# Optimization experiments

Measured on AMD Instinct MI355X. Metric: run time of the kernel, lower is better.

The kernel has to match this reference:

```python
import jax, jax.numpy as jnp
import numpy as np

S = 4096   # decoder sequence length
T = 4096   # encoder sequence length
D = 2048   # x_size == qk_size (required for q @ k^T to typecheck)


def setup_inputs() -> dict:
    key = jax.random.key(0)
    k1, k2, k3, k4 = jax.random.split(key, 4)
    x_vectors = jax.random.normal(k1, (S, D), dtype=jnp.float32)
    enc_output = jax.random.normal(k2, (2, T, S), dtype=jnp.float32) * 0.02
    Wq = jax.random.normal(k3, (D, D), dtype=jnp.float32) * 0.02
    bq = jax.random.normal(k4, (D,), dtype=jnp.float32) * 0.02
    return {"x_vectors": x_vectors, "enc_output": enc_output, "Wq": Wq, "bq": bq}


def reference(x_vectors, enc_output, Wq, bq):
    # q = Linear(x): [S, D]
    q = x_vectors @ Wq.T + bq
    # k, v produced by matmul of encoder-output matrices with x: [T, D]
    k = enc_output[0] @ x_vectors
    v = enc_output[1] @ x_vectors
    # attention scores [S, T], scaled by sqrt(qk_size)
    e = (q @ k.T) / jnp.sqrt(jnp.float32(D))
    # softmax over dim=1 (last axis of the rank-2 score matrix)
    a = jax.nn.softmax(e, axis=1)
    # z = a @ v^T: [S, D]
    z = a @ v
    return z
```

## Files before the change

### kernel.cpp

```cpp
#include <hip/hip_runtime.h>


typedef __attribute__((ext_vector_type(8))) __bf16 bf16x8;
typedef __attribute__((ext_vector_type(4))) float f32x4;
typedef __attribute__((ext_vector_type(4))) unsigned short ushort4v;
typedef __attribute__((ext_vector_type(8))) unsigned short ushort8v;

#define S_DIM 4096
#define T_DIM 4096
#define D_DIM 2048

__device__ __forceinline__ unsigned short f2bf(float f) {
    unsigned int u = __float_as_uint(f);
    u += 0x7fffu + ((u >> 16) & 1u);
    return (unsigned short)(u >> 16);
}

__device__ __forceinline__ void block_sync() {
    __builtin_amdgcn_sched_barrier(0);
    __builtin_amdgcn_s_barrier();
    __builtin_amdgcn_sched_barrier(0);
}

#define GL(gptr, sptr)                                                        \
    __builtin_amdgcn_global_load_lds(                                         \
        (__attribute__((address_space(1))) void*)(void*)(gptr),               \
        (__attribute__((address_space(3))) void*)(sptr), 16, 0, 0)

__device__ __forceinline__ f32x4 MFMA(bf16x8 a, bf16x8 b, f32x4 c) {
    return __builtin_amdgcn_mfma_f32_16x16x32_bf16(a, b, c, 0, 0, 0);
}

__global__ __launch_bounds__(256)
void k_convert(const float* __restrict__ in, unsigned short* __restrict__ out, long n) {
    long i = ((long)blockIdx.x * blockDim.x + threadIdx.x) * 8;
    const long stride = (long)gridDim.x * blockDim.x * 8;
    for (; i < n; i += stride) {
        float4 a = *(const float4*)(in + i);
        float4 b = *(const float4*)(in + i + 4);
        ushort8v o;
        o[0] = f2bf(a.x); o[1] = f2bf(a.y); o[2] = f2bf(a.z); o[3] = f2bf(a.w);
        o[4] = f2bf(b.x); o[5] = f2bf(b.y); o[6] = f2bf(b.z); o[7] = f2bf(b.w);
        *(ushort8v*)(out + i) = o;
    }
}

__global__ __launch_bounds__(256)
void k_transpose(const float* __restrict__ in, unsigned short* __restrict__ out,
                 int R, int C) {
    __shared__ float tile[32][33];
    const int bx = blockIdx.x * 32;
    const int by = blockIdx.y * 32;
    const int tx = threadIdx.x;
    const int ty = threadIdx.y;
    #pragma unroll
    for (int i = 0; i < 32; i += 8)
        tile[ty + i][tx] = in[(long)(by + ty + i) * C + bx + tx];
    __syncthreads();
    #pragma unroll
    for (int i = 0; i < 32; i += 8)
        out[(long)(bx + ty + i) * R + by + tx] = f2bf(tile[tx][ty + i]);
}

__global__ __launch_bounds__(256)
void k_transpose_bf(const unsigned short* __restrict__ in,
                    unsigned short* __restrict__ out, int R, int C) {
    __shared__ unsigned short tile[32][33];
    const int bx = blockIdx.x * 32;
    const int by = blockIdx.y * 32;
    const int tx = threadIdx.x;
    const int ty = threadIdx.y;
    #pragma unroll
    for (int i = 0; i < 32; i += 8)
        tile[ty + i][tx] = in[(long)(by + ty + i) * C + bx + tx];
    __syncthreads();
    #pragma unroll
    for (int i = 0; i < 32; i += 8)
        out[(long)(bx + ty + i) * R + by + tx] = tile[tx][ty + i];
}

template<int MFR, bool DOSTG, bool DOREAD, int WVM, bool DOBAR, int LPTA>
__device__ __forceinline__ void seg_t(
    const unsigned short* (&gA)[2], const int (&ldA)[2],
    const unsigned short* (&gB)[2], const int (&ldB)[2],
    char* cur, char* nxt, char* stg, int arB, int brB,
    bf16x8 (&au)[4], bf16x8 (&bu)[4], bf16x8 (&af)[4], bf16x8 (&bf_)[4],
    f32x4 (&acc)[MFR][4])
{
    bf16x8 a47[4];
    if constexpr (MFR == 8) {
        #pragma unroll
        for (int j = 0; j < 4; ++j)
            a47[j] = *(const bf16x8*)(cur + arB + (4 + j) * 1024);
    }
    if constexpr (DOSTG) {
        #pragma unroll
        for (int j = 0; j < LPTA; ++j) { GL(gA[j], stg + ldA[j]); gA[j] += 32; }
        #pragma unroll
        for (int j = 0; j < 2; ++j)    { GL(gB[j], stg + ldB[j]); gB[j] += 32; }
    }
    if constexpr (DOREAD) {
        #pragma unroll
        for (int n = 0; n < 4; ++n)
            bf_[n] = *(const bf16x8*)(nxt + brB + n * 1024);
        #pragma unroll
        for (int m = 0; m < 4; ++m)
            af[m] = *(const bf16x8*)(nxt + arB + m * 1024);
    }
    if constexpr (MFR == 8 && DOREAD)  asm volatile("s_waitcnt lgkmcnt(12)" ::: "memory");
    else if constexpr (MFR == 8)       asm volatile("s_waitcnt lgkmcnt(4)" ::: "memory");
    else if constexpr (DOREAD)         asm volatile("s_waitcnt lgkmcnt(8)" ::: "memory");
    else                               asm volatile("s_waitcnt lgkmcnt(0)" ::: "memory");
    __builtin_amdgcn_sched_barrier(0);
    __builtin_amdgcn_s_setprio(1);
    #pragma unroll
    for (int m = 0; m < 4; ++m)
        #pragma unroll
        for (int n = 0; n < 4; ++n)
            acc[m][n] = MFMA(au[m], bu[n], acc[m][n]);
    if constexpr (MFR == 8) {
        if constexpr (DOREAD) asm volatile("s_waitcnt lgkmcnt(8)" ::: "memory");
        else                  asm volatile("s_waitcnt lgkmcnt(0)" ::: "memory");
        __builtin_amdgcn_sched_barrier(0);
        #pragma unroll
        for (int j = 0; j < 4; ++j)
            #pragma unroll
            for (int n = 0; n < 4; ++n)
                acc[4 + j][n] = MFMA(a47[j], bu[n], acc[4 + j][n]);
    }
    __builtin_amdgcn_s_setprio(0);
    if constexpr (WVM == 4)      asm volatile("s_waitcnt vmcnt(4)" ::: "memory");
    else if constexpr (WVM == 3) asm volatile("s_waitcnt vmcnt(3)" ::: "memory");
    else if constexpr (WVM == 0) asm volatile("s_waitcnt vmcnt(0)" ::: "memory");
    if constexpr (DOBAR) block_sync();
}

template<int MFR, int OUT_BF16, int HAS_BIAS>
__global__ __launch_bounds__(512, 2)
void k_gemm(const unsigned short* __restrict__ A,
            const unsigned short* __restrict__ B,
            const float* __restrict__ bias,
            void* __restrict__ C,
            int M, int N, int K, float alpha) {
    constexpr int BM    = MFR * 32;
    constexpr int AGRAN = BM * 4;
    constexpr int LPTA  = AGRAN / 512;
    constexpr int LDSA  = AGRAN * 16;
    constexpr int SLOT  = LDSA + 16384;
    constexpr int LPT   = LPTA + 2;
    extern __shared__ __align__(16) char smem[];

    const int tid = threadIdx.x;
    const int l = tid & 63;
    const int w = tid >> 6;
    const int wr = w >> 2;
    const int wc = w & 3;

    const int gx = gridDim.x, gy = gridDim.y;
    const int flat = blockIdx.y * gx + blockIdx.x;
    const int per = (gx * gy) >> 3;
    const int wid = (flat & 7) * per + (flat >> 3);
    const int sc = wid / (gy * 4);
    const int rm = wid - sc * gy * 4;
    const int by = rm >> 2;
    const int bx = sc * 4 + (rm & 3);

    const long brow = (long)by * BM;
    const long bcol = (long)bx * 256;
    const int NT = K >> 5;

    const unsigned short* gA[2];
    int ldA[2];
    #pragma unroll
    for (int j = 0; j < LPTA; ++j) {
        const int q = (w * LPTA + j) * 64 + l;
        const int R = q >> 3, s = q & 7, cp = s ^ (R & 7);
        gA[j] = A + (brow + 2 * R + (cp & 1)) * (long)K + (cp >> 1) * 8;
        ldA[j] = q * 16;
    }
    const unsigned short* gB[2];
    int ldB[2];
    #pragma unroll
    for (int j = 0; j < 2; ++j) {
        const int q = (w * 2 + j) * 64 + l;
        const int R = q >> 3, s = q & 7, cp = s ^ (R & 7);
        gB[j] = B + (bcol + 2 * R + (cp & 1)) * (long)K + (cp >> 1) * 8;
        ldB[j] = LDSA + q * 16;
    }

    const int sAB = ((((l >> 4) << 1) | (l & 1)) ^ ((l & 15) >> 1)) << 4;
    const int arB = (wr * (MFR * 8) + ((l & 15) >> 1)) * 128 + sAB;
    const int brB = LDSA + (wc * 32 + ((l & 15) >> 1)) * 128 + sAB;

    char* P0 = smem;
    char* P1 = smem + SLOT;
    char* P2 = smem + 2 * SLOT;
    char* P3 = smem + 3 * SLOT;

    f32x4 acc[MFR][4] = {};
    bf16x8 aE[4], bE[4], aO[4], bO[4];

    {
        auto stage = [&](char* dst) {
            #pragma unroll
            for (int j = 0; j < LPTA; ++j) { GL(gA[j], dst + ldA[j]); gA[j] += 32; }
            #pragma unroll
            for (int j = 0; j < 2; ++j)    { GL(gB[j], dst + ldB[j]); gB[j] += 32; }
        };
        stage(P0); stage(P1); stage(P2);
        if constexpr (MFR == 8) asm volatile("s_waitcnt vmcnt(4)" ::: "memory");
        else                    asm volatile("s_waitcnt vmcnt(3)" ::: "memory");
        block_sync();
        #pragma unroll
        for (int n = 0; n < 4; ++n) bE[n] = *(const bf16x8*)(P0 + brB + n * 1024);
        #pragma unroll
        for (int m = 0; m < 4; ++m) aE[m] = *(const bf16x8*)(P0 + arB + m * 1024);
    }

    constexpr int WVM = (MFR == 8) ? 4 : 3;
    for (int t = 0; t + 6 <= NT; t += 2) {
        seg_t<MFR, true, true, WVM, true, LPTA>(gA, ldA, gB, ldB, P0, P1, P3,
                                                arB, brB, aE, bE, aO, bO, acc);
        seg_t<MFR, true, true, WVM, true, LPTA>(gA, ldA, gB, ldB, P1, P2, P0,
                                                arB, brB, aO, bO, aE, bE, acc);
        char* tp = P0; P0 = P2; P2 = tp;
        tp = P1; P1 = P3; P3 = tp;
    }
    seg_t<MFR, true,  true, WVM, true, LPTA>(gA, ldA, gB, ldB, P0, P1, P3,
                                             arB, brB, aE, bE, aO, bO, acc);
    seg_t<MFR, false, true, 0,   true, LPTA>(gA, ldA, gB, ldB, P1, P2, nullptr,
                                             arB, brB, aO, bO, aE, bE, acc);
    seg_t<MFR, false, true, -1,  true, LPTA>(gA, ldA, gB, ldB, P2, P3, nullptr,
                                             arB, brB, aE, bE, aO, bO, acc);
    seg_t<MFR, false, false, -1, false, LPTA>(gA, ldA, gB, ldB, P3, nullptr, nullptr,
                                              arB, brB, aO, bO, aE, bE, acc);

    const long crow0 = brow + wr * (MFR * 16) + (l >> 4) * 4;
    const long ccol0 = bcol + wc * 64 + (l & 15);
    #pragma unroll
    for (int n = 0; n < 4; ++n) {
        const long col = ccol0 + n * 16;
        const float bb = HAS_BIAS ? bias[col] : 0.0f;
        #pragma unroll
        for (int m = 0; m < MFR; ++m) {
            #pragma unroll
            for (int r = 0; r < 4; ++r) {
                const long row = crow0 + m * 16 + r;
                const float v = acc[m][n][r] * alpha + bb;
                if (OUT_BF16)
                    ((unsigned short*)C)[row * N + col] = f2bf(v);
                else
                    ((float*)C)[row * N + col] = v;
            }
        }
    }
}

__global__ __launch_bounds__(256)
void k_softmax(const float* __restrict__ E, unsigned short* __restrict__ A, int T) {
    const long row = blockIdx.x;
    const float* er = E + row * (long)T;
    const int t = threadIdx.x;
    const int l = t & 63;
    const int w = t >> 6;

    float4 v[4];
    float m = -3.4e38f;
    #pragma unroll
    for (int j = 0; j < 4; ++j) {
        v[j] = *(const float4*)(er + j * 1024 + t * 4);
        m = fmaxf(m, fmaxf(fmaxf(v[j].x, v[j].y), fmaxf(v[j].z, v[j].w)));
    }
    #pragma unroll
    for (int o = 32; o > 0; o >>= 1) m = fmaxf(m, __shfl_xor(m, o));

    __shared__ float redm[4];
    __shared__ float reds[4];
    if (l == 0) redm[w] = m;
    __syncthreads();
    m = fmaxf(fmaxf(redm[0], redm[1]), fmaxf(redm[2], redm[3]));

    float s = 0.f;
    #pragma unroll
    for (int j = 0; j < 4; ++j) {
        v[j].x = __expf(v[j].x - m); s += v[j].x;
        v[j].y = __expf(v[j].y - m); s += v[j].y;
        v[j].z = __expf(v[j].z - m); s += v[j].z;
        v[j].w = __expf(v[j].w - m); s += v[j].w;
    }
    #pragma unroll
    for (int o = 32; o > 0; o >>= 1) s += __shfl_xor(s, o);
    if (l == 0) reds[w] = s;
    __syncthreads();
    s = reds[0] + reds[1] + reds[2] + reds[3];
    const float inv = 1.0f / s;

    unsigned short* ar = A + row * (long)T;
    #pragma unroll
    for (int j = 0; j < 4; ++j) {
        ushort4v o4;
        o4[0] = f2bf(v[j].x * inv);
        o4[1] = f2bf(v[j].y * inv);
        o4[2] = f2bf(v[j].z * inv);
        o4[3] = f2bf(v[j].w * inv);
        *(ushort4v*)(ar + j * 1024 + t * 4) = o4;
    }
}

extern "C" void kernel_launch(void* const* d_in, const int* in_sizes, int n_in,
                              void* d_out, int out_size, void* d_ws, size_t ws_size,
                              hipStream_t stream) {
    const float* x   = (const float*)d_in[0];
    const float* enc = (const float*)d_in[1];
    const float* Wq  = (const float*)d_in[2];
    const float* bq  = (const float*)d_in[3];
    float* out = (float*)d_out;
    char* ws = (char*)d_ws;

    unsigned short* abf   = (unsigned short*)(ws);
    unsigned short* xT    = (unsigned short*)(ws);
    unsigned short* xbf   = (unsigned short*)(ws + (16L << 20));
    unsigned short* wqbf  = (unsigned short*)(ws + (32L << 20));
    unsigned short* qbf   = (unsigned short*)(ws + (40L << 20));
    unsigned short* kv    = (unsigned short*)(ws + (56L << 20));
    unsigned short* vT    = (unsigned short*)(ws + (88L << 20));
    unsigned short* encbf = (unsigned short*)(ws + (104L << 20));
    float*          e     = (float*)(ws + (104L << 20));

    k_convert<<<4096, 256, 0, stream>>>(x,   xbf,   (long)S_DIM * D_DIM);
    k_convert<<<4096, 256, 0, stream>>>(Wq,  wqbf,  (long)D_DIM * D_DIM);
    k_convert<<<4096, 256, 0, stream>>>(enc, encbf, 2L * T_DIM * S_DIM);
    k_transpose<<<dim3(D_DIM / 32, S_DIM / 32), dim3(32, 8), 0, stream>>>(x, xT, S_DIM, D_DIM);

    #define LAUNCH_G(MFRV, OB, HB, Ap, Bp, biasp, Cp, M_, N_, K_, al)                      \
        do {                                                                               \
            constexpr int smemB = ((MFRV * 32 * 4) * 16 + 16384) * 4;                      \
            hipFuncSetAttribute((const void*)k_gemm<MFRV, OB, HB>,                         \
                                hipFuncAttributeMaxDynamicSharedMemorySize, smemB);        \
            k_gemm<MFRV, OB, HB><<<dim3((N_) / 256, (M_) / (MFRV * 32)), 512, smemB,       \
                                   stream>>>(Ap, Bp, biasp, Cp, M_, N_, K_, al);           \
        } while (0)

    LAUNCH_G(4, 1, 1, xbf, wqbf, bq, qbf, S_DIM, D_DIM, D_DIM, 1.0f);
    LAUNCH_G(8, 1, 0, encbf, xT, nullptr, kv, 2 * T_DIM, D_DIM, S_DIM, 1.0f);
    k_transpose_bf<<<dim3(D_DIM / 32, T_DIM / 32), dim3(32, 8), 0, stream>>>(
        kv + (long)T_DIM * D_DIM, vT, T_DIM, D_DIM);
    LAUNCH_G(8, 0, 0, qbf, kv, nullptr, e, S_DIM, T_DIM, D_DIM, 0.022097086912079608f);
    k_softmax<<<S_DIM, 256, 0, stream>>>(e, abf, T_DIM);
    LAUNCH_G(4, 0, 0, abf, vT, nullptr, out, S_DIM, D_DIM, T_DIM, 1.0f);
}
```

Before: 391.4 us.

## Load GEMM B operand directly from global into registers, bypassing LDS

Each wave now loads its B fragments straight from global memory into registers with a two-step lookahead, instead of staging B tiles through shared memory. Only the A tile is still staged in LDS, so shared memory per block shrinks and the B LDS writes and reads plus their waits go away. The vmcnt and lgkmcnt accounting is retuned to match. In exchange, B loads are no longer shared across waves, which duplicates global/L2 traffic, and the direct loads are less coalesced and their latency is exposed in registers.

```diff
diff --git a/kernel.cpp b/kernel.cpp
--- a/kernel.cpp
+++ b/kernel.cpp
@@ -79,12 +79,12 @@
         out[(long)(bx + ty + i) * R + by + tx] = tile[tx][ty + i];
 }
 
-template<int MFR, bool DOSTG, bool DOREAD, int WVM, bool DOBAR, int LPTA>
+template<int MFR, bool DOSTG, bool DOB, int WVM, bool DOBAR, bool DOREAD, int LPTA>
 __device__ __forceinline__ void seg_t(
     const unsigned short* (&gA)[2], const int (&ldA)[2],
-    const unsigned short* (&gB)[2], const int (&ldB)[2],
-    char* cur, char* nxt, char* stg, int arB, int brB,
-    bf16x8 (&au)[4], bf16x8 (&bu)[4], bf16x8 (&af)[4], bf16x8 (&bf_)[4],
+    const unsigned short* const (&gB)[4],
+    char* cur, char* nxt, char* stg, int arB, long kOffB,
+    bf16x8 (&au)[4], bf16x8 (&af)[4], bf16x8 (&bu)[4],
     f32x4 (&acc)[MFR][4])
 {
     bf16x8 a47[4];
@@ -93,24 +93,18 @@
         for (int j = 0; j < 4; ++j)
             a47[j] = *(const bf16x8*)(cur + arB + (4 + j) * 1024);
     }
-    if constexpr (DOSTG) {
-        #pragma unroll
-        for (int j = 0; j < LPTA; ++j) { GL(gA[j], stg + ldA[j]); gA[j] += 32; }
-        #pragma unroll
-        for (int j = 0; j < 2; ++j)    { GL(gB[j], stg + ldB[j]); gB[j] += 32; }
-    }
     if constexpr (DOREAD) {
-        #pragma unroll
-        for (int n = 0; n < 4; ++n)
-            bf_[n] = *(const bf16x8*)(nxt + brB + n * 1024);
         #pragma unroll
         for (int m = 0; m < 4; ++m)
             af[m] = *(const bf16x8*)(nxt + arB + m * 1024);
     }
-    if constexpr (MFR == 8 && DOREAD)  asm volatile("s_waitcnt lgkmcnt(12)" ::: "memory");
-    else if constexpr (MFR == 8)       asm volatile("s_waitcnt lgkmcnt(4)" ::: "memory");
-    else if constexpr (DOREAD)         asm volatile("s_waitcnt lgkmcnt(8)" ::: "memory");
-    else                               asm volatile("s_waitcnt lgkmcnt(0)" ::: "memory");
+    if constexpr (MFR == 8) {
+        if constexpr (DOREAD) asm volatile("s_waitcnt lgkmcnt(8)" ::: "memory");
+        else                  asm volatile("s_waitcnt lgkmcnt(4)" ::: "memory");
+    } else {
+        if constexpr (DOREAD) asm volatile("s_waitcnt lgkmcnt(4)" ::: "memory");
+        else                  asm volatile("s_waitcnt lgkmcnt(0)" ::: "memory");
+    }
     __builtin_amdgcn_sched_barrier(0);
     __builtin_amdgcn_s_setprio(1);
     #pragma unroll
@@ -119,7 +113,7 @@
         for (int n = 0; n < 4; ++n)
             acc[m][n] = MFMA(au[m], bu[n], acc[m][n]);
     if constexpr (MFR == 8) {
-        if constexpr (DOREAD) asm volatile("s_waitcnt lgkmcnt(8)" ::: "memory");
+        if constexpr (DOREAD) asm volatile("s_waitcnt lgkmcnt(4)" ::: "memory");
         else                  asm volatile("s_waitcnt lgkmcnt(0)" ::: "memory");
         __builtin_amdgcn_sched_barrier(0);
         #pragma unroll
@@ -129,8 +123,18 @@
                 acc[4 + j][n] = MFMA(a47[j], bu[n], acc[4 + j][n]);
     }
     __builtin_amdgcn_s_setprio(0);
-    if constexpr (WVM == 4)      asm volatile("s_waitcnt vmcnt(4)" ::: "memory");
-    else if constexpr (WVM == 3) asm volatile("s_waitcnt vmcnt(3)" ::: "memory");
+    if constexpr (DOB) {
+        #pragma unroll
+        for (int n = 0; n < 4; ++n)
+            bu[n] = *(const bf16x8*)(gB[n] + kOffB);
+    }
+    if constexpr (DOSTG) {
+        #pragma unroll
+        for (int j = 0; j < LPTA; ++j) { GL(gA[j], stg + ldA[j]); gA[j] += 32; }
+    }
+    if constexpr (WVM == 6)      asm volatile("s_waitcnt vmcnt(6)" ::: "memory");
+    else if constexpr (WVM == 5) asm volatile("s_waitcnt vmcnt(5)" ::: "memory");
+    else if constexpr (WVM == 4) asm volatile("s_waitcnt vmcnt(4)" ::: "memory");
     else if constexpr (WVM == 0) asm volatile("s_waitcnt vmcnt(0)" ::: "memory");
     if constexpr (DOBAR) block_sync();
 }
@@ -145,9 +149,7 @@
     constexpr int BM    = MFR * 32;
     constexpr int AGRAN = BM * 4;
     constexpr int LPTA  = AGRAN / 512;
-    constexpr int LDSA  = AGRAN * 16;
-    constexpr int SLOT  = LDSA + 16384;
-    constexpr int LPT   = LPTA + 2;
+    constexpr int SLOT  = AGRAN * 16;
     extern __shared__ __align__(16) char smem[];
 
     const int tid = threadIdx.x;
@@ -178,19 +180,13 @@
         gA[j] = A + (brow + 2 * R + (cp & 1)) * (long)K + (cp >> 1) * 8;
         ldA[j] = q * 16;
     }
-    const unsigned short* gB[2];
-    int ldB[2];
-    #pragma unroll
-    for (int j = 0; j < 2; ++j) {
-        const int q = (w * 2 + j) * 64 + l;
-        const int R = q >> 3, s = q & 7, cp = s ^ (R & 7);
-        gB[j] = B + (bcol + 2 * R + (cp & 1)) * (long)K + (cp >> 1) * 8;
-        ldB[j] = LDSA + q * 16;
-    }
+    const unsigned short* gB[4];
+    #pragma unroll
+    for (int n = 0; n < 4; ++n)
+        gB[n] = B + (bcol + wc * 64 + n * 16 + (l & 15)) * (long)K + (l >> 4) * 8;
 
     const int sAB = ((((l >> 4) << 1) | (l & 1)) ^ ((l & 15) >> 1)) << 4;
     const int arB = (wr * (MFR * 8) + ((l & 15) >> 1)) * 128 + sAB;
-    const int brB = LDSA + (wc * 32 + ((l & 15) >> 1)) * 128 + sAB;
 
     char* P0 = smem;
     char* P1 = smem + SLOT;
@@ -198,42 +194,44 @@
     char* P3 = smem + 3 * SLOT;
 
     f32x4 acc[MFR][4] = {};
-    bf16x8 aE[4], bE[4], aO[4], bO[4];
+    bf16x8 aE[4], aO[4], bE[4], bO[4];
 
     {
-        auto stage = [&](char* dst) {
+        char* d = smem;
+        #pragma unroll
+        for (int tt = 0; tt < 3; ++tt) {
             #pragma unroll
-            for (int j = 0; j < LPTA; ++j) { GL(gA[j], dst + ldA[j]); gA[j] += 32; }
-            #pragma unroll
-            for (int j = 0; j < 2; ++j)    { GL(gB[j], dst + ldB[j]); gB[j] += 32; }
-        };
-        stage(P0); stage(P1); stage(P2);
-        if constexpr (MFR == 8) asm volatile("s_waitcnt vmcnt(4)" ::: "memory");
-        else                    asm volatile("s_waitcnt vmcnt(3)" ::: "memory");
+            for (int j = 0; j < LPTA; ++j) { GL(gA[j], d + ldA[j]); gA[j] += 32; }
+            d += SLOT;
+        }
+        __builtin_amdgcn_sched_barrier(0);
+        #pragma unroll
+        for (int n = 0; n < 4; ++n) bE[n] = *(const bf16x8*)(gB[n]);
+        #pragma unroll
+        for (int n = 0; n < 4; ++n) bO[n] = *(const bf16x8*)(gB[n] + 32);
+        asm volatile("s_waitcnt vmcnt(4)" ::: "memory");
         block_sync();
         #pragma unroll
-        for (int n = 0; n < 4; ++n) bE[n] = *(const bf16x8*)(P0 + brB + n * 1024);
-        #pragma unroll
         for (int m = 0; m < 4; ++m) aE[m] = *(const bf16x8*)(P0 + arB + m * 1024);
     }
 
-    constexpr int WVM = (MFR == 8) ? 4 : 3;
+    constexpr int WST = 4 + LPTA;
     for (int t = 0; t + 6 <= NT; t += 2) {
-        seg_t<MFR, true, true, WVM, true, LPTA>(gA, ldA, gB, ldB, P0, P1, P3,
-                                                arB, brB, aE, bE, aO, bO, acc);
-        seg_t<MFR, true, true, WVM, true, LPTA>(gA, ldA, gB, ldB, P1, P2, P0,
-                                                arB, brB, aO, bO, aE, bE, acc);
+        seg_t<MFR, true, true, WST, true, true, LPTA>(
+            gA, ldA, gB, P0, P1, P3, arB, (long)(t + 2) << 5, aE, aO, bE, acc);
+        seg_t<MFR, true, true, WST, true, true, LPTA>(
+            gA, ldA, gB, P1, P2, P0, arB, (long)(t + 3) << 5, aO, aE, bO, acc);
         char* tp = P0; P0 = P2; P2 = tp;
         tp = P1; P1 = P3; P3 = tp;
     }
-    seg_t<MFR, true,  true, WVM, true, LPTA>(gA, ldA, gB, ldB, P0, P1, P3,
-                                             arB, brB, aE, bE, aO, bO, acc);
-    seg_t<MFR, false, true, 0,   true, LPTA>(gA, ldA, gB, ldB, P1, P2, nullptr,
-                                             arB, brB, aO, bO, aE, bE, acc);
-    seg_t<MFR, false, true, -1,  true, LPTA>(gA, ldA, gB, ldB, P2, P3, nullptr,
-                                             arB, brB, aE, bE, aO, bO, acc);
-    seg_t<MFR, false, false, -1, false, LPTA>(gA, ldA, gB, ldB, P3, nullptr, nullptr,
-                                              arB, brB, aO, bO, aE, bE, acc);
+    seg_t<MFR, true,  true,  WST, true, true, LPTA>(
+        gA, ldA, gB, P0, P1, P3, arB, (long)(NT - 2) << 5, aE, aO, bE, acc);
+    seg_t<MFR, false, true,  4,   true, true, LPTA>(
+        gA, ldA, gB, P1, P2, P0, arB, (long)(NT - 1) << 5, aO, aE, bO, acc);
+    seg_t<MFR, false, false, 0,   true, true, LPTA>(
+        gA, ldA, gB, P2, P3, P1, arB, 0, aE, aO, bE, acc);
+    seg_t<MFR, false, false, -1,  false, false, LPTA>(
+        gA, ldA, gB, P3, P0, P2, arB, 0, aO, aE, bO, acc);
 
     const long crow0 = brow + wr * (MFR * 16) + (l >> 4) * 4;
     const long ccol0 = bcol + wc * 64 + (l & 15);
@@ -334,7 +332,7 @@
 
     #define LAUNCH_G(MFRV, OB, HB, Ap, Bp, biasp, Cp, M_, N_, K_, al)                      \
         do {                                                                               \
-            constexpr int smemB = ((MFRV * 32 * 4) * 16 + 16384) * 4;                      \
+            constexpr int smemB = (MFRV * 32 * 64) * 4;                                    \
             hipFuncSetAttribute((const void*)k_gemm<MFRV, OB, HB>,                         \
                                 hipFuncAttributeMaxDynamicSharedMemorySize, smemB);        \
             k_gemm<MFRV, OB, HB><<<dim3((N_) / 256, (M_) / (MFRV * 32)), 512, smemB,       \
```

Result: slower. 546.4 us (+39.6%).
